# Kernel tuning notes

Measured on AMD Instinct MI355X. Metric: run time of the kernel, lower is better.

Reference implementation:

```python
import jax, jax.numpy as jnp
import numpy as np

D = 1024      # input_dim
H = 4096      # expert_hidden_dim
C = 512       # num_classes
E = 8         # num_experts
K = 2         # top_k
B = 16384     # batch
LN_EPS = 1e-5


def setup_inputs() -> dict:
    key = jax.random.key(0)
    ks = jax.random.split(key, 6)
    scale = 0.02
    return {
        "x": jax.random.normal(ks[0], (B, D), dtype=jnp.float32),
        "gate_w": jax.random.normal(ks[1], (D, E), dtype=jnp.float32) * scale,
        "gate_b": jnp.zeros((E,), dtype=jnp.float32),
        "w1": jax.random.normal(ks[2], (E, D, H), dtype=jnp.float32) * scale,
        "b1": jnp.zeros((E, H), dtype=jnp.float32),
        "ln_g": jnp.ones((E, H), dtype=jnp.float32),
        "ln_b": jnp.zeros((E, H), dtype=jnp.float32),
        "w2": jax.random.normal(ks[3], (E, H, C), dtype=jnp.float32) * scale,
        "b2": jnp.zeros((E, C), dtype=jnp.float32),
    }


def reference(x, gate_w, gate_b, w1, b1, ln_g, ln_b, w2, b2):
    # Router: logits [B,E], top-k over experts, softmax over the k selected logits
    logits = x @ gate_w + gate_b
    top_vals, top_idx = jax.lax.top_k(logits, K)        # [B,K]
    probs = jax.nn.softmax(top_vals, axis=1)            # [B,K]

    # Combined gate weight per (token, expert): replaces the nested k/expert
    # mask-gather-scatter loops; top_idx rows have distinct experts, so this
    # is exactly sum_k probs[:,k] * (top_idx[:,k]==e). [B,E]
    n = x.shape[0]
    weight = jnp.zeros((n, E), dtype=x.dtype).at[jnp.arange(n)[:, None], top_idx].add(probs)

    out = jnp.zeros((n, C), dtype=x.dtype)
    for e in range(E):  # fixed small expert count; each expert has distinct params
        h = x @ w1[e] + b1[e]                           # [B,H]
        mu = jnp.mean(h, axis=-1, keepdims=True)
        var = jnp.var(h, axis=-1, keepdims=True)
        h = (h - mu) * jax.lax.rsqrt(var + LN_EPS) * ln_g[e] + ln_b[e]
        h = jax.nn.gelu(h, approximate=False)           # torch GELU default = erf
        # Dropout is identity in eval mode.
        out = out + weight[:, e:e + 1] * (h @ w2[e] + b2[e])
    return out, logits
```

## Files before the change

### kernel.cpp

```cpp
#include <hip/hip_runtime.h>
#include <hip/hip_bf16.h>
#include <cstdint>

#define DEV __device__ __forceinline__

constexpr int Bt = 16384;
constexpr int Dd = 1024;
constexpr int Hh = 4096;
constexpr int Cc = 512;
constexpr int Ee = 8;
constexpr int PCAP = 34816;

typedef short bf16x8 __attribute__((ext_vector_type(8)));
typedef ushort u16x8 __attribute__((ext_vector_type(8)));
typedef float f32x4  __attribute__((ext_vector_type(4)));

DEV ushort f2bf(float f){
  uint32_t u = __float_as_uint(f);
  u += 0x7fffu + ((u >> 16) & 1u);
  return (ushort)(u >> 16);
}
DEV float bf2f(ushort u){ return __uint_as_float(((uint32_t)u) << 16); }

DEV float gelu_t(float x){
  float x2 = x * x;
  float z = x * (0.7978845608f + 0.0356774081f * x2);
  float t = __builtin_amdgcn_exp2f(z * -2.8853900818f);
  return x * __builtin_amdgcn_rcpf(1.f + t);
}

typedef const __attribute__((address_space(1))) void* gptr_t;
typedef __attribute__((address_space(3))) void* lptr_t;
DEV void gload_lds16(const void* g, void* l){
  __builtin_amdgcn_global_load_lds((gptr_t)g, (lptr_t)l, 16, 0, 0);
}

#define BARRIER() __builtin_amdgcn_s_barrier()
#define WAITL(N) do { asm volatile("s_waitcnt lgkmcnt(" #N ")" ::: "memory"); \
                      __builtin_amdgcn_sched_barrier(0); } while(0)
#define WAITV(N) asm volatile("s_waitcnt vmcnt(" #N ")" ::: "memory")

__global__ __launch_bounds__(256) void k_routercvt(
    const float* __restrict__ x, const float* __restrict__ gw,
    const float* __restrict__ gb, float* __restrict__ logits,
    int2* __restrict__ topi, float2* __restrict__ topp, ushort* __restrict__ xb)
{
  __shared__ float lgwT[Ee * Dd];
  int tid = threadIdx.x;
  const float4* gw4 = (const float4*)gw;
  for (int i = tid; i < Dd * Ee / 4; i += 256){
    float4 v = gw4[i];
    int d = i >> 1, e0 = (i & 1) * 4;
    lgwT[(e0 + 0) * Dd + d] = v.x;
    lgwT[(e0 + 1) * Dd + d] = v.y;
    lgwT[(e0 + 2) * Dd + d] = v.z;
    lgwT[(e0 + 3) * Dd + d] = v.w;
  }
  __syncthreads();
  int wv = tid >> 6, lane = tid & 63;
  int t = blockIdx.x * 4 + wv;
  const float4* xr4 = (const float4*)(x + (size_t)t * Dd);
  ushort* xbr = xb + (size_t)t * Dd;
  float acc[Ee];
  #pragma unroll
  for (int e = 0; e < Ee; e++) acc[e] = 0.f;
  #pragma unroll
  for (int i = 0; i < 4; i++){
    int d4 = i * 256 + lane * 4;
    float4 xs = xr4[d4 >> 2];
    ushort4 o; o.x = f2bf(xs.x); o.y = f2bf(xs.y); o.z = f2bf(xs.z); o.w = f2bf(xs.w);
    *(ushort4*)(xbr + d4) = o;
    #pragma unroll
    for (int e = 0; e < Ee; e++){
      float4 wv4 = *(const float4*)(lgwT + e * Dd + d4);
      acc[e] += xs.x * wv4.x + xs.y * wv4.y + xs.z * wv4.z + xs.w * wv4.w;
    }
  }
  #pragma unroll
  for (int e = 0; e < Ee; e++){
    #pragma unroll
    for (int m = 1; m < 64; m <<= 1) acc[e] += __shfl_xor(acc[e], m, 64);
  }
  if (lane == 0){
    float lg[Ee];
    #pragma unroll
    for (int e = 0; e < Ee; e++) lg[e] = acc[e] + gb[e];
    #pragma unroll
    for (int e = 0; e < Ee; e++) logits[(size_t)t * Ee + e] = lg[e];
    int i0 = 0; float v0 = lg[0];
    #pragma unroll
    for (int e = 1; e < Ee; e++) if (lg[e] > v0){ v0 = lg[e]; i0 = e; }
    int i1 = (i0 == 0) ? 1 : 0; float v1 = lg[i1];
    #pragma unroll
    for (int e = 0; e < Ee; e++) if (e != i0 && lg[e] > v1){ v1 = lg[e]; i1 = e; }
    float ex = expf(v1 - v0);
    float p0 = 1.f / (1.f + ex);
    float p1 = ex * p0;
    topi[t] = make_int2(i0, i1);
    topp[t] = make_float2(p0, p1);
  }
}

__global__ __launch_bounds__(256) void k_offsets(
    const int2* __restrict__ topi, int* __restrict__ off)
{
  __shared__ int part[4][8];
  int tid = threadIdx.x, lane = tid & 63, w = tid >> 6;
  int c0 = 0, c1 = 0, c2 = 0, c3 = 0, c4 = 0, c5 = 0, c6 = 0, c7 = 0;
  for (int t = tid; t < Bt; t += 256){
    int2 ii = topi[t];
    c0 += (ii.x == 0) + (ii.y == 0);
    c1 += (ii.x == 1) + (ii.y == 1);
    c2 += (ii.x == 2) + (ii.y == 2);
    c3 += (ii.x == 3) + (ii.y == 3);
    c4 += (ii.x == 4) + (ii.y == 4);
    c5 += (ii.x == 5) + (ii.y == 5);
    c6 += (ii.x == 6) + (ii.y == 6);
    c7 += (ii.x == 7) + (ii.y == 7);
  }
  #pragma unroll
  for (int m = 1; m < 64; m <<= 1){
    c0 += __shfl_xor(c0, m, 64); c1 += __shfl_xor(c1, m, 64);
    c2 += __shfl_xor(c2, m, 64); c3 += __shfl_xor(c3, m, 64);
    c4 += __shfl_xor(c4, m, 64); c5 += __shfl_xor(c5, m, 64);
    c6 += __shfl_xor(c6, m, 64); c7 += __shfl_xor(c7, m, 64);
  }
  if (lane == 0){
    part[w][0] = c0; part[w][1] = c1; part[w][2] = c2; part[w][3] = c3;
    part[w][4] = c4; part[w][5] = c5; part[w][6] = c6; part[w][7] = c7;
  }
  __syncthreads();
  if (tid == 0){
    int a = 0;
    for (int e = 0; e < Ee; e++){
      int h = part[0][e] + part[1][e] + part[2][e] + part[3][e];
      off[e] = a; a += ((h + 255) >> 8) << 8;
    }
    off[Ee] = a;
  }
}

__global__ __launch_bounds__(256) void k_scatter(
    const int2* __restrict__ topi, const int* __restrict__ off,
    int* __restrict__ fill, int* __restrict__ ptok, int2* __restrict__ pidx)
{
  __shared__ int lcnt[8], lbase[8];
  int tid = threadIdx.x;
  if (tid < 8) lcnt[tid] = 0;
  __syncthreads();
  int t = blockIdx.x * 256 + tid;
  int2 ii = topi[t];
  int r0 = atomicAdd(&lcnt[ii.x], 1);
  int r1 = atomicAdd(&lcnt[ii.y], 1);
  __syncthreads();
  if (tid < 8) lbase[tid] = off[tid] + atomicAdd(&fill[tid], lcnt[tid]);
  __syncthreads();
  int p0 = lbase[ii.x] + r0;
  int p1 = lbase[ii.y] + r1;
  ptok[p0] = t;
  ptok[p1] = t;
  pidx[t] = make_int2(p0, p1);
}

__global__ __launch_bounds__(256) void k_transpose_bf16(
    const float* __restrict__ in, ushort* __restrict__ outp, int R, int Cd)
{
  __shared__ float tl[64][65];
  size_t eoff = (size_t)blockIdx.z * (size_t)R * (size_t)Cd;
  int c0 = blockIdx.x * 64, r0 = blockIdx.y * 64;
  int tid = threadIdx.x;
  int r = tid >> 2, cq = tid & 3;
  const float* src = in + eoff + (size_t)(r0 + r) * Cd + c0 + cq * 16;
  #pragma unroll
  for (int q = 0; q < 4; q++){
    float4 v = ((const float4*)src)[q];
    int cc = cq * 16 + q * 4;
    tl[r][cc + 0] = v.x; tl[r][cc + 1] = v.y; tl[r][cc + 2] = v.z; tl[r][cc + 3] = v.w;
  }
  __syncthreads();
  int c = tid >> 2, rq = tid & 3;
  ushort* dst = outp + eoff + (size_t)(c0 + c) * R + r0 + rq * 16;
  #pragma unroll
  for (int q = 0; q < 4; q++){
    ushort4 o;
    o.x = f2bf(tl[rq * 16 + q * 4 + 0][c]);
    o.y = f2bf(tl[rq * 16 + q * 4 + 1][c]);
    o.z = f2bf(tl[rq * 16 + q * 4 + 2][c]);
    o.w = f2bf(tl[rq * 16 + q * 4 + 3][c]);
    ((ushort4*)dst)[q] = o;
  }
}


DEV void read_Aq(bf16x8 (&aq)[4][2], const char* lb, int abase, const uint32_t (&alane)[2]){
  #pragma unroll
  for (int i = 0; i < 4; i++)
    #pragma unroll
    for (int k2 = 0; k2 < 2; k2++)
      aq[i][k2] = *(const bf16x8*)(lb + abase + i * 2048 + alane[k2]);
}
template<int P>
DEV void read_Bp(bf16x8 (&bq)[4][2], const char* lb, int wn, const uint32_t (&alane)[2]){
  #pragma unroll
  for (int j = 0; j < 2; j++)
    #pragma unroll
    for (int k2 = 0; k2 < 2; k2++)
      bq[P * 2 + j][k2] = *(const bf16x8*)(lb + 32768 + (wn >> 1) * 16384 +
                              (wn & 1) * 8192 + P * 4096 + j * 2048 + alane[k2]);
}
template<int MQ, int NB>
DEV void mfma_half(f32x4 (&acc)[8][4], const bf16x8 (&a)[4][2], const bf16x8 (&b)[4][2]){
  #pragma unroll
  for (int i = 0; i < 4; i++)
    #pragma unroll
    for (int j = 0; j < 2; j++)
      #pragma unroll
      for (int k2 = 0; k2 < 2; k2++)
        acc[MQ * 4 + i][NB * 2 + j] = __builtin_amdgcn_mfma_f32_16x16x32_bf16(
            a[i][k2], b[NB * 2 + j][k2], acc[MQ * 4 + i][NB * 2 + j], 0, 0, 0);
}
DEV void stage4(const char* gb, const uint32_t (&src)[2][2], uint32_t ko, char* dst){
  gload_lds16(gb + src[0][0] + ko, dst);
  gload_lds16(gb + src[0][1] + ko, dst + 8192);
  gload_lds16(gb + src[1][0] + ko, dst + 16384);
  gload_lds16(gb + src[1][1] + ko, dst + 16384 + 8192);
}

template<int MODE, int Kd, int Nd, int KS>
__global__ __launch_bounds__(512, 2) void k_gemm8(
    const ushort* __restrict__ A, const ushort* __restrict__ Bm,
    const float* __restrict__ bias, const int* __restrict__ off,
    const int* __restrict__ ptok, ushort* __restrict__ Outp, int chunk_base,
    int plane_elems)
{
  __shared__ char lds[131072];
  constexpr int Kh  = Kd / KS;
  constexpr int NTk = Kh / 64;
  constexpr int NTn = Nd / 256;
  int nwg = gridDim.x;
  int orig = blockIdx.x;
  int q = nwg >> 3, r8 = nwg & 7;
  int xcd = orig & 7, lin = orig >> 3;
  int swz = (xcd < r8 ? xcd * (q + 1) : r8 * (q + 1) + (xcd - r8) * q) + lin;
  int inner = swz % (NTn * KS);
  int m = swz / (NTn * KS);
  int nI = inner % NTn, ksI = inner / NTn;
  int r0l = m * 256;
  int n0 = nI * 256;
  uint32_t kbyte = (uint32_t)ksI * (uint32_t)(Kh * 2);
  int grow0 = chunk_base + r0l;
  if (grow0 >= off[8]) return;

  int tid = threadIdx.x;
  int e = 0;
  #pragma unroll
  for (int i = 1; i < 8; i++) e = (grow0 >= off[i]) ? i : e;

  uint32_t sx = (uint32_t)(((tid & 7) ^ ((tid >> 3) & 7)) << 4);
  int rh0 = tid >> 3, rh1 = rh0 + 64;
  uint32_t a_src[2][2], b_src[2][2];
  #pragma unroll
  for (int h = 0; h < 2; h++){
    int ra0 = h * 128 + rh0, ra1 = h * 128 + rh1;
    uint32_t rowb0, rowb1;
    if (MODE == 0){
      rowb0 = (uint32_t)ptok[grow0 + ra0] * (uint32_t)(Kd * 2);
      rowb1 = (uint32_t)ptok[grow0 + ra1] * (uint32_t)(Kd * 2);
    } else {
      rowb0 = (uint32_t)(r0l + ra0) * (uint32_t)(Kd * 2);
      rowb1 = (uint32_t)(r0l + ra1) * (uint32_t)(Kd * 2);
    }
    a_src[h][0] = rowb0 + kbyte + sx;
    a_src[h][1] = rowb1 + kbyte + sx;
    b_src[h][0] = (uint32_t)(e * Nd + n0 + ra0) * (uint32_t)(Kd * 2) + kbyte + sx;
    b_src[h][1] = (uint32_t)(e * Nd + n0 + ra1) * (uint32_t)(Kd * 2) + kbyte + sx;
  }
  const char* Ab = (const char*)A;
  const char* Bb = (const char*)Bm;
  int w = tid >> 6, lane = tid & 63;
  int wm = w >> 2, wn = w & 3;
  int l15 = lane & 15, lhi = lane >> 4;
  char* wdst = lds + w * 1024;
  int abase0 = wm * 16384;
  int abase1 = wm * 16384 + 8192;

  uint32_t alane[2];
  #pragma unroll
  for (int k2 = 0; k2 < 2; k2++)
    alane[k2] = (uint32_t)(l15 * 128 + (((k2 * 4 + lhi) ^ (l15 & 7)) << 4));

  f32x4 acc[8][4];
  #pragma unroll
  for (int mi = 0; mi < 8; mi++)
    #pragma unroll
    for (int ni = 0; ni < 4; ni++) acc[mi][ni] = (f32x4){0.f, 0.f, 0.f, 0.f};
  bf16x8 aq[4][2], bq[4][2];

  stage4(Ab, a_src, 0u, wdst);
  stage4(Bb, b_src, 0u, wdst + 32768);
  stage4(Ab, a_src, 128u, wdst + 65536);
  stage4(Bb, b_src, 128u, wdst + 65536 + 32768);
  WAITV(8);
  BARRIER();
  read_Aq(aq, lds, abase0, alane);
  read_Bp<0>(bq, lds, wn, alane);
  read_Bp<1>(bq, lds, wn, alane);

  #pragma unroll 1
  for (int t = 0; t < NTk; ++t){
    const char* lb = lds + (t & 1) * 65536;
    char* wlb = wdst + (t & 1) * 65536;
    WAITL(4);
    __builtin_amdgcn_s_setprio(1);
    mfma_half<0, 0>(acc, aq, bq);
    __builtin_amdgcn_s_setprio(0);
    WAITL(0);
    __builtin_amdgcn_s_setprio(1);
    mfma_half<0, 1>(acc, aq, bq);
    __builtin_amdgcn_s_setprio(0);
    read_Aq(aq, lb, abase1, alane);
    WAITL(0);
    BARRIER();
    if (t + 2 < NTk){
      uint32_t ko2 = (uint32_t)(t + 2) * 128u;
      stage4(Ab, a_src, ko2, wlb);
      stage4(Bb, b_src, ko2, wlb + 32768);
    }
    __builtin_amdgcn_s_setprio(1);
    mfma_half<1, 1>(acc, aq, bq);
    mfma_half<1, 0>(acc, aq, bq);
    __builtin_amdgcn_s_setprio(0);
    if (t + 2 < NTk)      { WAITV(8); }
    else if (t + 1 < NTk) { WAITV(0); }
    BARRIER();
    if (t + 1 < NTk){
      const char* nb = lds + ((t + 1) & 1) * 65536;
      read_Aq(aq, nb, abase0, alane);
      read_Bp<0>(bq, nb, wn, alane);
      read_Bp<1>(bq, nb, wn, alane);
    }
  }

  float bv[4]; int nn[4];
  #pragma unroll
  for (int ni = 0; ni < 4; ni++){
    nn[ni] = n0 + wn * 64 + ni * 16 + l15;
    bv[ni] = (MODE == 0 || ksI == 0) ? bias[e * Nd + nn[ni]] : 0.f;
  }
  ushort* OutP = Outp + (size_t)ksI * (size_t)plane_elems;
  #pragma unroll
  for (int mi = 0; mi < 8; mi++){
    #pragma unroll
    for (int r = 0; r < 4; r++){
      int rl = r0l + wm * 128 + mi * 16 + lhi * 4 + r;
      size_t rowbase = (MODE == 0) ? (size_t)rl * Nd
                                   : (size_t)(chunk_base + rl) * Nd;
      #pragma unroll
      for (int ni = 0; ni < 4; ni++){
        float v = acc[mi][ni][r] + bv[ni];
        OutP[rowbase + nn[ni]] = f2bf(v);
      }
    }
  }
}

__global__ __launch_bounds__(256) void k_lngelu(
    ushort* __restrict__ h, const int* __restrict__ off,
    const float* __restrict__ lng, const float* __restrict__ lnb, int chunk_base)
{
  __shared__ float redS[8];
  int rl = blockIdx.x, tid = threadIdx.x;
  int grow = chunk_base + rl;
  if (grow >= off[8]) return;
  int e = 0;
  #pragma unroll
  for (int i = 1; i < 8; i++) e = (grow >= off[i]) ? i : e;
  ushort* hr = h + (size_t)rl * Hh;
  float xv[16];
  #pragma unroll
  for (int i = 0; i < 4; i++){
    int c = i * 256 + tid;
    ushort4 v = *(const ushort4*)(hr + c * 4);
    xv[i * 4 + 0] = bf2f(v.x); xv[i * 4 + 1] = bf2f(v.y);
    xv[i * 4 + 2] = bf2f(v.z); xv[i * 4 + 3] = bf2f(v.w);
  }
  float s0 = 0.f, s1 = 0.f;
  #pragma unroll
  for (int i = 0; i < 16; i++){ s0 += xv[i]; s1 += xv[i] * xv[i]; }
  #pragma unroll
  for (int m = 1; m < 64; m <<= 1){ s0 += __shfl_xor(s0, m, 64); s1 += __shfl_xor(s1, m, 64); }
  int w = tid >> 6;
  if ((tid & 63) == 0){ redS[w * 2] = s0; redS[w * 2 + 1] = s1; }
  __syncthreads();
  s0 = redS[0] + redS[2] + redS[4] + redS[6];
  s1 = redS[1] + redS[3] + redS[5] + redS[7];
  float mu = s0 * (1.f / 4096.f);
  float var = s1 * (1.f / 4096.f) - mu * mu;
  float rs = rsqrtf(var + 1e-5f);
  const float4* gp = (const float4*)(lng + (size_t)e * Hh);
  const float4* bp = (const float4*)(lnb + (size_t)e * Hh);
  #pragma unroll
  for (int i = 0; i < 4; i++){
    int c = i * 256 + tid;
    float4 g = gp[c], b = bp[c];
    float v0 = (xv[i * 4 + 0] - mu) * rs * g.x + b.x;
    float v1 = (xv[i * 4 + 1] - mu) * rs * g.y + b.y;
    float v2 = (xv[i * 4 + 2] - mu) * rs * g.z + b.z;
    float v3 = (xv[i * 4 + 3] - mu) * rs * g.w + b.w;
    ushort4 o;
    o.x = f2bf(gelu_t(v0)); o.y = f2bf(gelu_t(v1));
    o.z = f2bf(gelu_t(v2)); o.w = f2bf(gelu_t(v3));
    *(ushort4*)(hr + c * 4) = o;
  }
}

__global__ __launch_bounds__(128) void k_combine(
    const ushort* __restrict__ y, int plane, const int2* __restrict__ pidx,
    const float2* __restrict__ topp, float* __restrict__ outp)
{
  int t = blockIdx.x;
  int c4 = threadIdx.x << 2;
  int2 pi = pidx[t]; float2 pp = topp[t];
  ushort4 a0 = *(const ushort4*)(y + (size_t)pi.x * Cc + c4);
  ushort4 a1 = *(const ushort4*)(y + (size_t)plane + (size_t)pi.x * Cc + c4);
  ushort4 b0 = *(const ushort4*)(y + (size_t)pi.y * Cc + c4);
  ushort4 b1 = *(const ushort4*)(y + (size_t)plane + (size_t)pi.y * Cc + c4);
  float4 o;
  o.x = pp.x * (bf2f(a0.x) + bf2f(a1.x)) + pp.y * (bf2f(b0.x) + bf2f(b1.x));
  o.y = pp.x * (bf2f(a0.y) + bf2f(a1.y)) + pp.y * (bf2f(b0.y) + bf2f(b1.y));
  o.z = pp.x * (bf2f(a0.z) + bf2f(a1.z)) + pp.y * (bf2f(b0.z) + bf2f(b1.z));
  o.w = pp.x * (bf2f(a0.w) + bf2f(a1.w)) + pp.y * (bf2f(b0.w) + bf2f(b1.w));
  *(float4*)(outp + (size_t)t * Cc + c4) = o;
}

extern "C" void kernel_launch(void* const* d_in, const int* in_sizes, int n_in,
                              void* d_out, int out_size, void* d_ws, size_t ws_size,
                              hipStream_t stream)
{
  const float* x   = (const float*)d_in[0];
  const float* gw  = (const float*)d_in[1];
  const float* gb  = (const float*)d_in[2];
  const float* w1  = (const float*)d_in[3];
  const float* b1  = (const float*)d_in[4];
  const float* lng = (const float*)d_in[5];
  const float* lnb = (const float*)d_in[6];
  const float* w2  = (const float*)d_in[7];
  const float* b2  = (const float*)d_in[8];
  float* outp   = (float*)d_out;
  float* logits = outp + (size_t)Bt * Cc;

  constexpr int YPLANE = PCAP * Cc;

  char* p = (char*)d_ws;
  auto alloc = [&](size_t bytes) -> char* {
    char* q = p; p += (bytes + 255) & ~(size_t)255; return q;
  };
  int*    ctrl  = (int*)alloc(256);
  int* fill = ctrl + 8; int* off = ctrl + 16;
  int2*   topi  = (int2*)alloc((size_t)Bt * 8);
  float2* topp  = (float2*)alloc((size_t)Bt * 8);
  int2*   pidx  = (int2*)alloc((size_t)Bt * 8);
  int*    ptok  = (int*)alloc((size_t)PCAP * 4);
  ushort* ybuf  = (ushort*)alloc((size_t)YPLANE * 2 * 2);
  ushort* xb    = (ushort*)alloc((size_t)Bt * Dd * 2);
  ushort* w1t   = (ushort*)alloc((size_t)Ee * Hh * Dd * 2);
  ushort* w2t   = (ushort*)alloc((size_t)Ee * Cc * Hh * 2);
  size_t used  = (size_t)(p - (char*)d_ws);
  size_t avail = ws_size > used ? ws_size - used : 0;
  long long chr = (long long)(avail / ((size_t)Hh * 2));
  chr &= ~255LL;
  int CH = (int)(chr < 256 ? 256 : (chr > PCAP ? (long long)PCAP : chr));
  ushort* hbuf = (ushort*)p;

  hipMemsetAsync(ctrl, 0, 256, stream);
  hipMemsetAsync(ptok, 0, (size_t)PCAP * 4, stream);

  k_routercvt<<<Bt / 4, 256, 0, stream>>>(x, gw, gb, logits, topi, topp, xb);
  k_offsets<<<1, 256, 0, stream>>>(topi, off);
  k_scatter<<<Bt / 256, 256, 0, stream>>>(topi, off, fill, ptok, pidx);
  k_transpose_bf16<<<dim3(Hh / 64, Dd / 64, Ee), 256, 0, stream>>>(w1, w1t, Dd, Hh);
  k_transpose_bf16<<<dim3(Cc / 64, Hh / 64, Ee), 256, 0, stream>>>(w2, w2t, Hh, Cc);

  for (int base = 0; base < PCAP; base += CH){
    int rows = (PCAP - base < CH) ? (PCAP - base) : CH;
    int nb1 = (rows / 256) * (Hh / 256);
    k_gemm8<0, Dd, Hh, 1><<<nb1, 512, 0, stream>>>(xb, w1t, b1, off, ptok, hbuf, base, 0);
    k_lngelu<<<rows, 256, 0, stream>>>(hbuf, off, lng, lnb, base);
    int nb2 = (rows / 256) * (Cc / 256) * 2;
    k_gemm8<1, Hh, Cc, 2><<<nb2, 512, 0, stream>>>(hbuf, w2t, b2, off, ptok, ybuf, base, YPLANE);
  }
  k_combine<<<Bt, 128, 0, stream>>>(ybuf, YPLANE, pidx, topp, outp);
}
```

Baseline: 771.7 us.

## Interleave per-half global-to-LDS staging with MFMA phases in GEMM main loop

Restructures the double-buffered GEMM K-loop so global-to-LDS loads are issued in halves between the four MFMA quarter-phases. The A tile for the next step and the B tile two steps ahead are staged at different points, instead of all four tiles being issued at once after a barrier. This spreads memory traffic across the iteration and aims for finer-grained compute/load overlap. In exchange it adds more workgroup barriers per iteration and moves the fragment reads to the start of the loop, which can raise sync overhead and expose LDS read latency.

Measured after the change: 726.0 us (median of 2 runs). -5.9%, faster.

```diff
diff --git a/kernel.cpp b/kernel.cpp
--- a/kernel.cpp
+++ b/kernel.cpp
@@ -219,11 +219,9 @@
         acc[MQ * 4 + i][NB * 2 + j] = __builtin_amdgcn_mfma_f32_16x16x32_bf16(
             a[i][k2], b[NB * 2 + j][k2], acc[MQ * 4 + i][NB * 2 + j], 0, 0, 0);
 }
-DEV void stage4(const char* gb, const uint32_t (&src)[2][2], uint32_t ko, char* dst){
-  gload_lds16(gb + src[0][0] + ko, dst);
-  gload_lds16(gb + src[0][1] + ko, dst + 8192);
-  gload_lds16(gb + src[1][0] + ko, dst + 16384);
-  gload_lds16(gb + src[1][1] + ko, dst + 16384 + 8192);
+DEV void stage_half(const char* gb, const uint32_t* src2, uint32_t ko, char* dstbase){
+  gload_lds16(gb + src2[0] + ko, dstbase);
+  gload_lds16(gb + src2[1] + ko, dstbase + 8192);
 }
 
 template<int MODE, int Kd, int Nd, int KS>
@@ -280,7 +278,7 @@
   int w = tid >> 6, lane = tid & 63;
   int wm = w >> 2, wn = w & 3;
   int l15 = lane & 15, lhi = lane >> 4;
-  char* wdst = lds + w * 1024;
+  int wso = w * 1024;
   int abase0 = wm * 16384;
   int abase1 = wm * 16384 + 8192;
 
@@ -296,49 +294,55 @@
     for (int ni = 0; ni < 4; ni++) acc[mi][ni] = (f32x4){0.f, 0.f, 0.f, 0.f};
   bf16x8 aq[4][2], bq[4][2];
 
-  stage4(Ab, a_src, 0u, wdst);
-  stage4(Bb, b_src, 0u, wdst + 32768);
-  stage4(Ab, a_src, 128u, wdst + 65536);
-  stage4(Bb, b_src, 128u, wdst + 65536 + 32768);
-  WAITV(8);
+  stage_half(Ab, a_src[0], 0u, lds + 0     + wso);
+  stage_half(Ab, a_src[1], 0u, lds + 16384 + wso);
+  stage_half(Bb, b_src[0], 0u, lds + 32768 + wso);
+  stage_half(Bb, b_src[1], 0u, lds + 49152 + wso);
+  if (NTk > 1){
+    stage_half(Bb, b_src[0], 128u, lds + 65536 + 32768 + wso);
+    stage_half(Bb, b_src[1], 128u, lds + 65536 + 49152 + wso);
+    WAITV(4);
+  } else {
+    WAITV(0);
+  }
   BARRIER();
-  read_Aq(aq, lds, abase0, alane);
-  read_Bp<0>(bq, lds, wn, alane);
-  read_Bp<1>(bq, lds, wn, alane);
 
   #pragma unroll 1
   for (int t = 0; t < NTk; ++t){
     const char* lb = lds + (t & 1) * 65536;
-    char* wlb = wdst + (t & 1) * 65536;
-    WAITL(4);
+    char* nb = lds + ((t + 1) & 1) * 65536;
+    char* cb = lds + (t & 1) * 65536;
+    uint32_t ko1 = (uint32_t)(t + 1) * 128u;
+    uint32_t ko2 = (uint32_t)(t + 2) * 128u;
+    read_Aq(aq, lb, abase0, alane);
+    read_Bp<0>(bq, lb, wn, alane);
+    if (t + 1 < NTk) stage_half(Ab, a_src[0], ko1, nb + wso);
+    BARRIER(); WAITL(0);
     __builtin_amdgcn_s_setprio(1);
     mfma_half<0, 0>(acc, aq, bq);
     __builtin_amdgcn_s_setprio(0);
-    WAITL(0);
+    BARRIER();
+    read_Bp<1>(bq, lb, wn, alane);
+    if (t + 1 < NTk) stage_half(Ab, a_src[1], ko1, nb + 16384 + wso);
+    BARRIER(); WAITL(0);
     __builtin_amdgcn_s_setprio(1);
     mfma_half<0, 1>(acc, aq, bq);
     __builtin_amdgcn_s_setprio(0);
+    BARRIER();
     read_Aq(aq, lb, abase1, alane);
-    WAITL(0);
-    BARRIER();
-    if (t + 2 < NTk){
-      uint32_t ko2 = (uint32_t)(t + 2) * 128u;
-      stage4(Ab, a_src, ko2, wlb);
-      stage4(Bb, b_src, ko2, wlb + 32768);
-    }
+    if (t + 2 < NTk) stage_half(Bb, b_src[0], ko2, cb + 32768 + wso);
+    BARRIER(); WAITL(0);
     __builtin_amdgcn_s_setprio(1);
     mfma_half<1, 1>(acc, aq, bq);
+    __builtin_amdgcn_s_setprio(0);
+    BARRIER();
+    if (t + 2 < NTk) stage_half(Bb, b_src[1], ko2, cb + 49152 + wso);
+    __builtin_amdgcn_s_setprio(1);
     mfma_half<1, 0>(acc, aq, bq);
     __builtin_amdgcn_s_setprio(0);
-    if (t + 2 < NTk)      { WAITV(8); }
+    if (t + 2 < NTk)      { WAITV(4); }
     else if (t + 1 < NTk) { WAITV(0); }
     BARRIER();
-    if (t + 1 < NTk){
-      const char* nb = lds + ((t + 1) & 1) * 65536;
-      read_Aq(aq, nb, abase0, alane);
-      read_Bp<0>(bq, nb, wn, alane);
-      read_Bp<1>(bq, nb, wn, alane);
-    }
   }
 
   float bv[4]; int nn[4];
```

## Shrink expert GEMM tiles to 128x128 with 256-thread blocks

Applied to the files above, without the earlier changes.

The grouped expert GEMM moves from 256x256 tiles on 512-thread workgroups (128 KB LDS) to 128x128 tiles on 256-thread workgroups (64 KB LDS), with a 2x2 wave layout and four 16-row accumulator blocks per wave. The main loop is simplified: each iteration now reads all A/B fragments from the current LDS buffer up front and then issues the MFMAs, instead of prefetching the next tile's fragments in the middle of the compute. This is meant to launch many more, smaller workgroups and reduce register and LDS pressure per block. In exchange, arithmetic intensity per loaded byte halves, global and L2 traffic rises, and less LDS-read latency is hidden behind MFMA work.

Result: slower. 791.5 us (+2.6%).

```diff
diff --git a/kernel.cpp b/kernel.cpp
--- a/kernel.cpp
+++ b/kernel.cpp
@@ -192,51 +192,54 @@
 }
 
 
-DEV void read_Aq(bf16x8 (&aq)[4][2], const char* lb, int abase, const uint32_t (&alane)[2]){
-  #pragma unroll
-  for (int i = 0; i < 4; i++)
+DEV void read_A8(bf16x8 (&aq)[4][2], const char* buf, int wm, const uint32_t (&alane)[2]){
+  #pragma unroll
+  for (int mi = 0; mi < 4; mi++)
     #pragma unroll
     for (int k2 = 0; k2 < 2; k2++)
-      aq[i][k2] = *(const bf16x8*)(lb + abase + i * 2048 + alane[k2]);
+      aq[mi][k2] = *(const bf16x8*)(buf + wm * 8192 + mi * 2048 + alane[k2]);
 }
 template<int P>
-DEV void read_Bp(bf16x8 (&bq)[4][2], const char* lb, int wn, const uint32_t (&alane)[2]){
+DEV void read_B4(bf16x8 (&bq)[4][2], const char* buf, int wn, const uint32_t (&alane)[2]){
   #pragma unroll
   for (int j = 0; j < 2; j++)
     #pragma unroll
     for (int k2 = 0; k2 < 2; k2++)
-      bq[P * 2 + j][k2] = *(const bf16x8*)(lb + 32768 + (wn >> 1) * 16384 +
-                              (wn & 1) * 8192 + P * 4096 + j * 2048 + alane[k2]);
-}
-template<int MQ, int NB>
-DEV void mfma_half(f32x4 (&acc)[8][4], const bf16x8 (&a)[4][2], const bf16x8 (&b)[4][2]){
-  #pragma unroll
-  for (int i = 0; i < 4; i++)
+      bq[P * 2 + j][k2] = *(const bf16x8*)(buf + 16384 + wn * 8192 +
+                                           (P * 2 + j) * 2048 + alane[k2]);
+}
+template<int P>
+DEV void mfma16(f32x4 (&acc)[4][4], const bf16x8 (&aq)[4][2], const bf16x8 (&bq)[4][2]){
+  #pragma unroll
+  for (int mi = 0; mi < 4; mi++)
     #pragma unroll
     for (int j = 0; j < 2; j++)
       #pragma unroll
       for (int k2 = 0; k2 < 2; k2++)
-        acc[MQ * 4 + i][NB * 2 + j] = __builtin_amdgcn_mfma_f32_16x16x32_bf16(
-            a[i][k2], b[NB * 2 + j][k2], acc[MQ * 4 + i][NB * 2 + j], 0, 0, 0);
-}
-DEV void stage4(const char* gb, const uint32_t (&src)[2][2], uint32_t ko, char* dst){
-  gload_lds16(gb + src[0][0] + ko, dst);
-  gload_lds16(gb + src[0][1] + ko, dst + 8192);
-  gload_lds16(gb + src[1][0] + ko, dst + 16384);
-  gload_lds16(gb + src[1][1] + ko, dst + 16384 + 8192);
+        acc[mi][P * 2 + j] = __builtin_amdgcn_mfma_f32_16x16x32_bf16(
+            aq[mi][k2], bq[P * 2 + j][k2], acc[mi][P * 2 + j], 0, 0, 0);
+}
+DEV void stage8(const char* Ab, const char* Bb, const uint32_t (&a_src)[4],
+                const uint32_t (&b_src)[4], uint32_t ko, char* buf, int tid){
+  #pragma unroll
+  for (int g = 0; g < 4; g++)
+    gload_lds16(Ab + a_src[g] + ko, buf + g * 4096 + tid * 16);
+  #pragma unroll
+  for (int g = 0; g < 4; g++)
+    gload_lds16(Bb + b_src[g] + ko, buf + 16384 + g * 4096 + tid * 16);
 }
 
 template<int MODE, int Kd, int Nd, int KS>
-__global__ __launch_bounds__(512, 2) void k_gemm8(
+__global__ __launch_bounds__(256, 2) void k_gemm(
     const ushort* __restrict__ A, const ushort* __restrict__ Bm,
     const float* __restrict__ bias, const int* __restrict__ off,
     const int* __restrict__ ptok, ushort* __restrict__ Outp, int chunk_base,
     int plane_elems)
 {
-  __shared__ char lds[131072];
+  __shared__ char lds[65536];
   constexpr int Kh  = Kd / KS;
   constexpr int NTk = Kh / 64;
-  constexpr int NTn = Nd / 256;
+  constexpr int NTn = Nd / 128;
   int nwg = gridDim.x;
   int orig = blockIdx.x;
   int q = nwg >> 3, r8 = nwg & 7;
@@ -245,8 +248,8 @@
   int inner = swz % (NTn * KS);
   int m = swz / (NTn * KS);
   int nI = inner % NTn, ksI = inner / NTn;
-  int r0l = m * 256;
-  int n0 = nI * 256;
+  int r0l = m * 128;
+  int n0 = nI * 128;
   uint32_t kbyte = (uint32_t)ksI * (uint32_t)(Kh * 2);
   int grow0 = chunk_base + r0l;
   if (grow0 >= off[8]) return;
@@ -257,88 +260,63 @@
   for (int i = 1; i < 8; i++) e = (grow0 >= off[i]) ? i : e;
 
   uint32_t sx = (uint32_t)(((tid & 7) ^ ((tid >> 3) & 7)) << 4);
-  int rh0 = tid >> 3, rh1 = rh0 + 64;
-  uint32_t a_src[2][2], b_src[2][2];
-  #pragma unroll
-  for (int h = 0; h < 2; h++){
-    int ra0 = h * 128 + rh0, ra1 = h * 128 + rh1;
-    uint32_t rowb0, rowb1;
-    if (MODE == 0){
-      rowb0 = (uint32_t)ptok[grow0 + ra0] * (uint32_t)(Kd * 2);
-      rowb1 = (uint32_t)ptok[grow0 + ra1] * (uint32_t)(Kd * 2);
-    } else {
-      rowb0 = (uint32_t)(r0l + ra0) * (uint32_t)(Kd * 2);
-      rowb1 = (uint32_t)(r0l + ra1) * (uint32_t)(Kd * 2);
-    }
-    a_src[h][0] = rowb0 + kbyte + sx;
-    a_src[h][1] = rowb1 + kbyte + sx;
-    b_src[h][0] = (uint32_t)(e * Nd + n0 + ra0) * (uint32_t)(Kd * 2) + kbyte + sx;
-    b_src[h][1] = (uint32_t)(e * Nd + n0 + ra1) * (uint32_t)(Kd * 2) + kbyte + sx;
+  int rh = tid >> 3;
+  uint32_t a_src[4], b_src[4];
+  #pragma unroll
+  for (int g = 0; g < 4; g++){
+    int ra = g * 32 + rh;
+    uint32_t rowb;
+    if (MODE == 0) rowb = (uint32_t)ptok[grow0 + ra] * (uint32_t)(Kd * 2);
+    else           rowb = (uint32_t)(r0l + ra) * (uint32_t)(Kd * 2);
+    a_src[g] = rowb + kbyte + sx;
+    b_src[g] = (uint32_t)(e * Nd + n0 + ra) * (uint32_t)(Kd * 2) + kbyte + sx;
   }
   const char* Ab = (const char*)A;
   const char* Bb = (const char*)Bm;
   int w = tid >> 6, lane = tid & 63;
-  int wm = w >> 2, wn = w & 3;
+  int wm = w >> 1, wn = w & 1;
   int l15 = lane & 15, lhi = lane >> 4;
-  char* wdst = lds + w * 1024;
-  int abase0 = wm * 16384;
-  int abase1 = wm * 16384 + 8192;
 
   uint32_t alane[2];
   #pragma unroll
   for (int k2 = 0; k2 < 2; k2++)
     alane[k2] = (uint32_t)(l15 * 128 + (((k2 * 4 + lhi) ^ (l15 & 7)) << 4));
 
-  f32x4 acc[8][4];
-  #pragma unroll
-  for (int mi = 0; mi < 8; mi++)
+  f32x4 acc[4][4];
+  #pragma unroll
+  for (int mi = 0; mi < 4; mi++)
     #pragma unroll
     for (int ni = 0; ni < 4; ni++) acc[mi][ni] = (f32x4){0.f, 0.f, 0.f, 0.f};
   bf16x8 aq[4][2], bq[4][2];
 
-  stage4(Ab, a_src, 0u, wdst);
-  stage4(Bb, b_src, 0u, wdst + 32768);
-  stage4(Ab, a_src, 128u, wdst + 65536);
-  stage4(Bb, b_src, 128u, wdst + 65536 + 32768);
+  stage8(Ab, Bb, a_src, b_src, 0u,   lds,         tid);
+  stage8(Ab, Bb, a_src, b_src, 128u, lds + 32768, tid);
   WAITV(8);
   BARRIER();
-  read_Aq(aq, lds, abase0, alane);
-  read_Bp<0>(bq, lds, wn, alane);
-  read_Bp<1>(bq, lds, wn, alane);
 
   #pragma unroll 1
   for (int t = 0; t < NTk; ++t){
-    const char* lb = lds + (t & 1) * 65536;
-    char* wlb = wdst + (t & 1) * 65536;
+    const char* buf = lds + (t & 1) * 32768;
+    char* sbuf = lds + (t & 1) * 32768;
+    read_A8(aq, buf, wm, alane);
+    read_B4<0>(bq, buf, wn, alane);
+    read_B4<1>(bq, buf, wn, alane);
     WAITL(4);
     __builtin_amdgcn_s_setprio(1);
-    mfma_half<0, 0>(acc, aq, bq);
+    mfma16<0>(acc, aq, bq);
     __builtin_amdgcn_s_setprio(0);
     WAITL(0);
     __builtin_amdgcn_s_setprio(1);
-    mfma_half<0, 1>(acc, aq, bq);
+    mfma16<1>(acc, aq, bq);
     __builtin_amdgcn_s_setprio(0);
-    read_Aq(aq, lb, abase1, alane);
-    WAITL(0);
     BARRIER();
     if (t + 2 < NTk){
-      uint32_t ko2 = (uint32_t)(t + 2) * 128u;
-      stage4(Ab, a_src, ko2, wlb);
-      stage4(Bb, b_src, ko2, wlb + 32768);
+      stage8(Ab, Bb, a_src, b_src, (uint32_t)(t + 2) * 128u, sbuf, tid);
+      WAITV(8);
+    } else if (t + 1 < NTk){
+      WAITV(0);
     }
-    __builtin_amdgcn_s_setprio(1);
-    mfma_half<1, 1>(acc, aq, bq);
-    mfma_half<1, 0>(acc, aq, bq);
-    __builtin_amdgcn_s_setprio(0);
-    if (t + 2 < NTk)      { WAITV(8); }
-    else if (t + 1 < NTk) { WAITV(0); }
     BARRIER();
-    if (t + 1 < NTk){
-      const char* nb = lds + ((t + 1) & 1) * 65536;
-      read_Aq(aq, nb, abase0, alane);
-      read_Bp<0>(bq, nb, wn, alane);
-      read_Bp<1>(bq, nb, wn, alane);
-    }
   }
 
   float bv[4]; int nn[4];
@@ -349,10 +327,10 @@
   }
   ushort* OutP = Outp + (size_t)ksI * (size_t)plane_elems;
   #pragma unroll
-  for (int mi = 0; mi < 8; mi++){
+  for (int mi = 0; mi < 4; mi++){
     #pragma unroll
     for (int r = 0; r < 4; r++){
-      int rl = r0l + wm * 128 + mi * 16 + lhi * 4 + r;
+      int rl = r0l + wm * 64 + mi * 16 + lhi * 4 + r;
       size_t rowbase = (MODE == 0) ? (size_t)rl * Nd
                                    : (size_t)(chunk_base + rl) * Nd;
       #pragma unroll
@@ -483,11 +461,11 @@
 
   for (int base = 0; base < PCAP; base += CH){
     int rows = (PCAP - base < CH) ? (PCAP - base) : CH;
-    int nb1 = (rows / 256) * (Hh / 256);
-    k_gemm8<0, Dd, Hh, 1><<<nb1, 512, 0, stream>>>(xb, w1t, b1, off, ptok, hbuf, base, 0);
+    int nb1 = (rows / 128) * (Hh / 128);
+    k_gemm<0, Dd, Hh, 1><<<nb1, 256, 0, stream>>>(xb, w1t, b1, off, ptok, hbuf, base, 0);
     k_lngelu<<<rows, 256, 0, stream>>>(hbuf, off, lng, lnb, base);
-    int nb2 = (rows / 256) * (Cc / 256) * 2;
-    k_gemm8<1, Hh, Cc, 2><<<nb2, 512, 0, stream>>>(hbuf, w2t, b2, off, ptok, ybuf, base, YPLANE);
+    int nb2 = (rows / 128) * (Cc / 128) * 2;
+    k_gemm<1, Hh, Cc, 2><<<nb2, 256, 0, stream>>>(hbuf, w2t, b2, off, ptok, ybuf, base, YPLANE);
   }
   k_combine<<<Bt, 128, 0, stream>>>(ybuf, YPLANE, pidx, topp, outp);
 }
```
